# Kernel optimization log

Measured on AMD Instinct MI355X. Metric: run time of the kernel, lower is better.

Reference implementation:

```python
import jax, jax.numpy as jnp
import numpy as np

B, T, C = 4, 2048, 1024
HEADS = 16
HEAD_DIM = C // HEADS
WINDOW = 256


def setup_inputs() -> dict:
    key = jax.random.key(0)
    k1, k2, k3 = jax.random.split(key, 3)
    x = jax.random.normal(k1, (B, T, C), dtype=jnp.float32)
    # torch nn.Linear weights: [out_features, in_features]; scale like kaiming-uniform-ish
    W_qkv = jax.random.normal(k2, (3 * C, C), dtype=jnp.float32) * (1.0 / np.sqrt(C))
    W_proj = jax.random.normal(k3, (C, C), dtype=jnp.float32) * (1.0 / np.sqrt(C))
    return {"x": x, "W_qkv": W_qkv, "W_proj": W_proj}


def reference(x, W_qkv, W_proj):
    b, t, c = x.shape
    h, d = HEADS, HEAD_DIM
    qkv = x @ W_qkv.T  # [b,t,3c]
    q, k, v = jnp.split(qkv, 3, axis=-1)
    q = q.reshape(b, t, h, d).transpose(0, 2, 1, 3)  # [b,h,t,d]
    k = k.reshape(b, t, h, d).transpose(0, 2, 1, 3)
    v = v.reshape(b, t, h, d).transpose(0, 2, 1, 3)
    scale = 1.0 / jnp.sqrt(jnp.asarray(d, dtype=q.dtype))
    scores = jnp.einsum('bhqd,bhkd->bhqk', q, k) * scale  # [b,h,t,t]
    i = jnp.arange(t)[:, None]
    j = jnp.arange(t)[None, :]
    mask = (j <= i) & (j > i - WINDOW)  # sliding-window causal band
    scores = jnp.where(mask, scores, -jnp.inf)
    attn = jax.nn.softmax(scores, axis=-1)
    y = jnp.einsum('bhqk,bhkd->bhqd', attn, v)  # [b,h,t,d]
    y = y.transpose(0, 2, 1, 3).reshape(b, t, c)
    return y @ W_proj.T
```

## Files before the change

kernel.cpp:

```cpp
#include <hip/hip_runtime.h>
#include <hip/hip_bf16.h>
#include <math.h>

#define BB 4
#define TT 2048
#define CC 1024
#define HH 16
#define DD 64
#define WW 256
#define MM (BB*TT)
#define NX (MM*CC)
#define NQ (3*CC*CC)
#define NP (CC*CC)

typedef __bf16 bf16x8 __attribute__((ext_vector_type(8)));
typedef __bf16 bf16x4 __attribute__((ext_vector_type(4)));
typedef float  f32x4  __attribute__((ext_vector_type(4)));

__device__ __forceinline__ void async_cp16(const void* g, void* l) {
  __builtin_amdgcn_global_load_lds(
      (const __attribute__((address_space(1))) void*)g,
      (__attribute__((address_space(3))) void*)l, 16, 0, 0);
}

__device__ __forceinline__ unsigned short f2bf(float v) {
  __hip_bfloat16 h = __float2bfloat16(v);
  return *(unsigned short*)&h;
}

__device__ __forceinline__ size_t wpk_off(int n, int k) {
  return ((((size_t)(n >> 7) * 16 + (k >> 6)) * 16) +
          (((k >> 3) & 7) * 2 + ((n >> 6) & 1))) * 512 +
         (size_t)(n & 63) * 8 + (k & 7);
}

__global__ __launch_bounds__(256)
void prep(const float* __restrict__ x,
          const float* __restrict__ wq,
          const float* __restrict__ wp,
          unsigned short* __restrict__ wpk,
          unsigned short* __restrict__ Apk) {
  const int p = blockIdx.x;
  const int tid = threadIdx.x;
  if (p < 4096) {
    int i = (p * 256 + tid) * 4;
    const float* src; unsigned short* dst; int n, k;
    if (i < NQ) { src = wq + i; n = i >> 10; k = i & 1023; dst = wpk; }
    else {
      int j = i - NQ;
      src = wp + j; n = j >> 10; k = j & 1023; dst = wpk + NQ;
    }
    float4 v = *(const float4*)src;
    size_t off = wpk_off(n, k);
    dst[off + 0] = f2bf(v.x);
    dst[off + 1] = f2bf(v.y);
    dst[off + 2] = f2bf(v.z);
    dst[off + 3] = f2bf(v.w);
    return;
  }
  __shared__ __align__(16) unsigned short tile[64 * 72];
  const int pid = p - 4096;
  const int bm = pid & 127;
  const int bk = pid >> 7;
  const int tr = tid >> 4;
  const int tc = (tid & 15) * 4;
#pragma unroll
  for (int i = 0; i < 4; i++) {
    int row = i * 16 + tr;
    float4 v = *(const float4*)&x[(size_t)(bm * 64 + row) * 1024 + bk * 64 + tc];
    tile[row * 72 + tc + 0] = f2bf(v.x);
    tile[row * 72 + tc + 1] = f2bf(v.y);
    tile[row * 72 + tc + 2] = f2bf(v.z);
    tile[row * 72 + tc + 3] = f2bf(v.w);
  }
  __syncthreads();
  const int w = tid >> 6, lane = tid & 63;
  const int quad = lane >> 4, l15 = lane & 15;
#pragma unroll
  for (int f = 0; f < 2; f++) {
    bf16x8 fr = *(const bf16x8*)&tile[(w * 16 + l15) * 72 + f * 32 + quad * 8];
    *(bf16x8*)&Apk[(((size_t)(bm * 4 + w) * 32) + bk * 2 + f) * 512 + lane * 8] = fr;
  }
}

__global__ __launch_bounds__(256, 2)
void gemm_qkv(const unsigned short* __restrict__ Apk,
              const unsigned short* __restrict__ Bw,
              unsigned short* __restrict__ Qh,
              unsigned short* __restrict__ Kh,
              unsigned short* __restrict__ Vt) {
  __shared__ __align__(16) unsigned short Bs[4][8192];

  const int id   = blockIdx.x;
  const int xcd  = id & 7;
  const int slot = id >> 3;
  const int mloc = slot / 24;
  const int nloc = slot % 24;
  const int m0 = (xcd * 4 + mloc) * 256;
  const int n0 = nloc * 128;

  const int tid  = threadIdx.x;
  const int w    = tid >> 6;
  const int lane = tid & 63;
  const int quad = lane >> 4;
  const int l15  = lane & 15;

  f32x4 acc[4][8];
#pragma unroll
  for (int i = 0; i < 4; i++)
#pragma unroll
    for (int j = 0; j < 8; j++) acc[i][j] = (f32x4)0.0f;

  const unsigned short* abase =
      Apk + ((size_t)((m0 >> 4) + w * 4) * 32) * 512 + lane * 8;

  const unsigned short* wb = Bw + (size_t)(n0 >> 7) * (16 * 16 * 512);

  auto stageB = [&](int kt, unsigned short* bs) {
#pragma unroll
    for (int i = 0; i < 4; i++) {
      int idx = w + 4 * i;
      async_cp16(wb + ((size_t)kt * 16 + idx) * 512 + lane * 8,
                 &bs[idx * 512]);
    }
  };

  bf16x8 Af[3][4];
  auto loadA = [&](int g, bf16x8* fr) {
#pragma unroll
    for (int tm = 0; tm < 4; tm++)
      fr[tm] = *(const bf16x8*)(abase + ((size_t)(tm * 32 + g)) * 512);
  };

  loadA(0, Af[0]);
  loadA(1, Af[1]);
  stageB(0, Bs[0]);
  stageB(1, Bs[1]);
  stageB(2, Bs[2]);
  asm volatile("s_waitcnt vmcnt(0)" ::: "memory");
  __builtin_amdgcn_sched_barrier(0);
  asm volatile("s_barrier" ::: "memory");

#pragma unroll
  for (int s = 0; s < 16; s++) {
    const unsigned short* bs = Bs[s & 3];
    if (s + 3 < 16) stageB(s + 3, Bs[(s + 3) & 3]);
#pragma unroll
    for (int sub = 0; sub < 2; sub++) {
      const int g = s * 2 + sub;
      if (g + 2 < 32) loadA(g + 2, Af[(g + 2) % 3]);
      const bf16x8* af = Af[g % 3];
      __builtin_amdgcn_s_setprio(1);
#pragma unroll
      for (int tn = 0; tn < 8; tn++) {
        bf16x8 bfv = *(const bf16x8*)
            &bs[(sub * 4 + quad) * 1024 + (tn * 16 + l15) * 8];
#pragma unroll
        for (int tm = 0; tm < 4; tm++)
          acc[tm][tn] = __builtin_amdgcn_mfma_f32_16x16x32_bf16(
              af[tm], bfv, acc[tm][tn], 0, 0, 0);
      }
      __builtin_amdgcn_s_setprio(0);
    }
    asm volatile("s_waitcnt vmcnt(16) lgkmcnt(0)" ::: "memory");
    __builtin_amdgcn_sched_barrier(0);
    asm volatile("s_barrier" ::: "memory");
  }

  const int t3 = n0 >> 10;
  if (t3 == 0) {
#pragma unroll
    for (int tm = 0; tm < 4; tm++)
#pragma unroll
      for (int tn = 0; tn < 8; tn++) {
        int colb = n0 + tn * 16;
        int hh = (colb >> 6) & 15;
        int dd = (colb & 63) + l15;
#pragma unroll
        for (int r = 0; r < 4; r++) {
          int row = m0 + w * 64 + tm * 16 + quad * 4 + r;
          int b = row >> 11, tt = row & 2047;
          Qh[((size_t)((b * 16 + hh) * 2048 + tt)) * 64 + dd] =
              f2bf(acc[tm][tn][r] * 0.125f);
        }
      }
  } else if (t3 == 1) {
#pragma unroll
    for (int tm = 0; tm < 4; tm++)
#pragma unroll
      for (int tn = 0; tn < 8; tn++) {
        int colb = n0 + tn * 16;
        int hh = (colb >> 6) & 15;
        int dd = (colb & 63) + l15;
#pragma unroll
        for (int r = 0; r < 4; r++) {
          int row = m0 + w * 64 + tm * 16 + quad * 4 + r;
          int b = row >> 11, tt = row & 2047;
          Kh[((((size_t)(b * 16 + hh) * 32 + (tt >> 6)) * 8 + (dd >> 3)) * 512)
             + (tt & 63) * 8 + (dd & 7)] = f2bf(acc[tm][tn][r]);
        }
      }
  } else {
    unsigned short* T = &Bs[0][0] + w * 4608;
    const int b    = (m0 + w * 64) >> 11;
    const int tc_g = ((m0 & 2047) >> 6) + w;
    const int h0   = (n0 >> 6) & 15;
#pragma unroll
    for (int hp = 0; hp < 2; hp++) {
#pragma unroll
      for (int tnl = 0; tnl < 4; tnl++)
#pragma unroll
        for (int tm = 0; tm < 4; tm++)
#pragma unroll
          for (int r = 0; r < 4; r++)
            T[(tnl * 16 + l15) * 72 + tm * 16 + quad * 4 + r] =
                f2bf(acc[tm][hp * 4 + tnl][r]);
      asm volatile("s_waitcnt lgkmcnt(0)" ::: "memory");
      const size_t base =
          ((size_t)((b * 16 + h0 + hp) * 32 + tc_g)) * 4096;
#pragma unroll
      for (int j = 0; j < 8; j++) {
        bf16x8 v = *(const bf16x8*)&T[lane * 72 + j * 8];
        *(bf16x8*)&Vt[base + (size_t)j * 512 + lane * 8] = v;
      }
    }
  }
}

__global__ __launch_bounds__(256, 2)
void gemm_proj(const unsigned short* __restrict__ Apk,
               const unsigned short* __restrict__ Bw,
               float* __restrict__ Co) {
  __shared__ __align__(16) unsigned short Bs[4][8192];

  const int id   = blockIdx.x;
  const int xcd  = id & 7;
  const int slot = id >> 3;
  const int mloc = slot >> 3;
  const int nloc = slot & 7;
  const int m0 = (xcd * 8 + mloc) * 128;
  const int n0 = nloc * 128;

  const int tid  = threadIdx.x;
  const int w    = tid >> 6;
  const int lane = tid & 63;
  const int quad = lane >> 4;
  const int l15  = lane & 15;

  f32x4 acc[2][8];
#pragma unroll
  for (int i = 0; i < 2; i++)
#pragma unroll
    for (int j = 0; j < 8; j++) acc[i][j] = (f32x4)0.0f;

  const unsigned short* abase =
      Apk + ((size_t)((m0 >> 4) + w * 2) * 32) * 512 + lane * 8;

  const unsigned short* wb = Bw + (size_t)(n0 >> 7) * (16 * 16 * 512);

  auto stageB = [&](int kt, unsigned short* bs) {
#pragma unroll
    for (int i = 0; i < 4; i++) {
      int idx = w + 4 * i;
      async_cp16(wb + ((size_t)kt * 16 + idx) * 512 + lane * 8,
                 &bs[idx * 512]);
    }
  };

  bf16x8 Af[3][2];
  auto loadA = [&](int g, bf16x8* fr) {
#pragma unroll
    for (int tm = 0; tm < 2; tm++)
      fr[tm] = *(const bf16x8*)(abase + ((size_t)(tm * 32 + g)) * 512);
  };

  stageB(0, Bs[0]);
  stageB(1, Bs[1]);
  stageB(2, Bs[2]);
  loadA(0, Af[0]);
  loadA(1, Af[1]);
  asm volatile("s_waitcnt vmcnt(12)" ::: "memory");
  __builtin_amdgcn_sched_barrier(0);
  __builtin_amdgcn_s_barrier();

#pragma unroll
  for (int s = 0; s < 16; s++) {
    const unsigned short* bs = Bs[s & 3];
    unsigned short* bn = Bs[(s + 3) & 3];
#pragma unroll
    for (int ph = 0; ph < 4; ph++) {
      const int ksub = ph >> 1;
      const int th   = ph & 1;
      const int g    = s * 2 + ksub;
      bf16x8 bfv[4];
#pragma unroll
      for (int j = 0; j < 4; j++)
        bfv[j] = *(const bf16x8*)
            &bs[(ksub * 4 + quad) * 1024 + ((th * 4 + j) * 16 + l15) * 8];
      if (s + 3 < 16)
        async_cp16(wb + ((size_t)(s + 3) * 16 + (w + 4 * ph)) * 512 + lane * 8,
                   &bn[(w + 4 * ph) * 512]);
      if ((ph & 1) == 0 && g + 2 < 32) loadA(g + 2, Af[(g + 2) % 3]);
      __builtin_amdgcn_s_barrier();
      asm volatile("s_waitcnt lgkmcnt(0)" ::: "memory");
      __builtin_amdgcn_sched_barrier(0);
      const bf16x8* af = Af[g % 3];
      __builtin_amdgcn_s_setprio(1);
#pragma unroll
      for (int j = 0; j < 4; j++)
#pragma unroll
        for (int tm = 0; tm < 2; tm++)
          acc[tm][th * 4 + j] = __builtin_amdgcn_mfma_f32_16x16x32_bf16(
              af[tm], bfv[j], acc[tm][th * 4 + j], 0, 0, 0);
      __builtin_amdgcn_s_setprio(0);
      __builtin_amdgcn_sched_barrier(0);
      if (ph == 3 && s < 15) {
        if (s <= 12)      asm volatile("s_waitcnt vmcnt(16)" ::: "memory");
        else if (s == 13) asm volatile("s_waitcnt vmcnt(12)" ::: "memory");
        else              asm volatile("s_waitcnt vmcnt(8)"  ::: "memory");
        __builtin_amdgcn_sched_barrier(0);
      }
      __builtin_amdgcn_s_barrier();
    }
  }

#pragma unroll
  for (int tm = 0; tm < 2; tm++)
#pragma unroll
    for (int tn = 0; tn < 8; tn++)
#pragma unroll
      for (int r = 0; r < 4; r++) {
        int row = m0 + w * 32 + tm * 16 + quad * 4 + r;
        int col = n0 + tn * 16 + l15;
        Co[(size_t)row * 1024 + col] = acc[tm][tn][r];
      }
}

__global__ __launch_bounds__(256, 2)
void attn_mfma(const unsigned short* __restrict__ Qh,
               const unsigned short* __restrict__ Kh,
               const unsigned short* __restrict__ Vt,
               unsigned short* __restrict__ Ypk) {
  __shared__ __align__(16) unsigned short SH[40960];

  const int tid  = threadIdx.x;
  const int w    = tid >> 6;
  const int lane = tid & 63;
  const int quad = lane >> 4;
  const int l15  = lane & 15;

  const int vid  = blockIdx.y * 32 + blockIdx.x;
  const int v    = (vid & 7) * 256 + (vid >> 3);
  const int bh   = v >> 5;
  const int q0   = (v & 31) << 6;

  const int c0 = (q0 >= 256) ? 0 : (4 - (q0 >> 6));

  const unsigned short* Qg = Qh + ((size_t)bh * 2048 + q0) * 64;
  bf16x8 Qf[2];
#pragma unroll
  for (int fs = 0; fs < 2; fs++)
    Qf[fs] = *(const bf16x8*)(Qg + (w * 16 + l15) * 64 + fs * 32 + quad * 8);

  const unsigned short* Kg = Kh + (size_t)bh * 32 * 4096;
  const unsigned short* Vg = Vt + (size_t)bh * 32 * 4096;
  for (int ch = c0; ch < 5; ch++) {
    int tc = (q0 >> 6) - 4 + ch;
#pragma unroll
    for (int i = 0; i < 2; i++) {
      int kc = w * 2 + i;
      async_cp16(Kg + ((size_t)tc * 8 + kc) * 512 + lane * 8,
                 &SH[ch * 4096 + kc * 512]);
    }
  }
  for (int ch = c0; ch < 5; ch++) {
    int tc = (q0 >> 6) - 4 + ch;
#pragma unroll
    for (int i = 0; i < 2; i++) {
      int kc = w * 2 + i;
      async_cp16(Vg + ((size_t)tc * 8 + kc) * 512 + lane * 8,
                 &SH[20480 + ch * 4096 + kc * 512]);
    }
  }
  if (c0 == 0)      asm volatile("s_waitcnt vmcnt(10)" ::: "memory");
  else if (c0 == 1) asm volatile("s_waitcnt vmcnt(8)"  ::: "memory");
  else if (c0 == 2) asm volatile("s_waitcnt vmcnt(6)"  ::: "memory");
  else if (c0 == 3) asm volatile("s_waitcnt vmcnt(4)"  ::: "memory");
  else              asm volatile("s_waitcnt vmcnt(2)"  ::: "memory");
  __builtin_amdgcn_sched_barrier(0);
  asm volatile("s_barrier" ::: "memory");

  f32x4 S[5][4];
#pragma unroll
  for (int ch = 0; ch < 5; ch++)
#pragma unroll
    for (int tn = 0; tn < 4; tn++) S[ch][tn] = (f32x4)0.0f;

#pragma unroll
  for (int ch = 0; ch < 5; ch++) {
    if (ch < c0) continue;
#pragma unroll
    for (int ks = 0; ks < 2; ks++) {
      int kc = ks * 4 + quad;
#pragma unroll
      for (int tn = 0; tn < 4; tn++) {
        bf16x8 bk = *(const bf16x8*)
            &SH[ch * 4096 + kc * 512 + (tn * 16 + l15) * 8];
        S[ch][tn] = __builtin_amdgcn_mfma_f32_16x16x32_bf16(
            Qf[ks], bk, S[ch][tn], 0, 0, 0);
      }
    }
  }

  const int qb = q0 + w * 16 + quad * 4;
  if (c0 == 0) {
#pragma unroll
    for (int tn = 0; tn < 4; tn++) {
      int j = q0 - 256 + tn * 16 + l15;
#pragma unroll
      for (int r = 0; r < 4; r++)
        if (qb + r > j + (WW - 1)) S[0][tn][r] = -__builtin_inff();
    }
  }
#pragma unroll
  for (int tn = 0; tn < 4; tn++) {
    int j = q0 + tn * 16 + l15;
#pragma unroll
    for (int r = 0; r < 4; r++)
      if (j > qb + r) S[4][tn][r] = -__builtin_inff();
  }

  float mrow[4], lrow[4];
#pragma unroll
  for (int r = 0; r < 4; r++) mrow[r] = -__builtin_inff();
#pragma unroll
  for (int ch = 0; ch < 5; ch++) {
    if (ch < c0) continue;
#pragma unroll
    for (int tn = 0; tn < 4; tn++)
#pragma unroll
      for (int r = 0; r < 4; r++)
        mrow[r] = fmaxf(mrow[r], S[ch][tn][r]);
  }
#pragma unroll
  for (int off = 1; off < 16; off <<= 1)
#pragma unroll
    for (int r = 0; r < 4; r++)
      mrow[r] = fmaxf(mrow[r], __shfl_xor(mrow[r], off));

#pragma unroll
  for (int r = 0; r < 4; r++) lrow[r] = 0.0f;
#pragma unroll
  for (int ch = 0; ch < 5; ch++) {
    if (ch < c0) continue;
#pragma unroll
    for (int tn = 0; tn < 4; tn++)
#pragma unroll
      for (int r = 0; r < 4; r++) {
        float e = __expf(S[ch][tn][r] - mrow[r]);
        S[ch][tn][r] = e;
        lrow[r] += e;
      }
  }
#pragma unroll
  for (int off = 1; off < 16; off <<= 1)
#pragma unroll
    for (int r = 0; r < 4; r++) lrow[r] += __shfl_xor(lrow[r], off);

  asm volatile("s_waitcnt vmcnt(0)" ::: "memory");
  __builtin_amdgcn_sched_barrier(0);
  asm volatile("s_barrier" ::: "memory");

  f32x4 Oacc[4];
#pragma unroll
  for (int td = 0; td < 4; td++) Oacc[td] = (f32x4)0.0f;

#pragma unroll
  for (int ch = 0; ch < 5; ch++) {
    if (ch < c0) continue;
    unsigned short* Ps = SH + (ch & 1) * 4608;
#pragma unroll
    for (int tn = 0; tn < 4; tn++)
#pragma unroll
      for (int r = 0; r < 4; r++)
        Ps[(w * 16 + quad * 4 + r) * 68 + tn * 16 + l15] = f2bf(S[ch][tn][r]);
    asm volatile("s_waitcnt lgkmcnt(0)" ::: "memory");
#pragma unroll
    for (int ks = 0; ks < 2; ks++) {
      int off = (w * 16 + l15) * 68 + ks * 32 + quad * 8;
      bf16x4 plo = *(const bf16x4*)&Ps[off];
      bf16x4 phi = *(const bf16x4*)&Ps[off + 4];
      bf16x8 ap = __builtin_shufflevector(plo, phi, 0, 1, 2, 3, 4, 5, 6, 7);
      int kc = ks * 4 + quad;
#pragma unroll
      for (int td = 0; td < 4; td++) {
        bf16x8 bv = *(const bf16x8*)
            &SH[20480 + ch * 4096 + kc * 512 + (td * 16 + l15) * 8];
        Oacc[td] = __builtin_amdgcn_mfma_f32_16x16x32_bf16(
            ap, bv, Oacc[td], 0, 0, 0);
      }
    }
  }

  const int b = bh >> 4, h = bh & 15;
  float inv[4];
#pragma unroll
  for (int r = 0; r < 4; r++) inv[r] = 1.0f / lrow[r];
  unsigned short* Ot = SH + 10240;
#pragma unroll
  for (int td = 0; td < 4; td++)
#pragma unroll
    for (int r = 0; r < 4; r++)
      Ot[(w * 16 + quad * 4 + r) * 72 + td * 16 + l15] =
          f2bf(Oacc[td][r] * inv[r]);
  asm volatile("s_waitcnt lgkmcnt(0)" ::: "memory");
  const size_t rt = (size_t)((b * 2048 + q0) >> 4) + w;
#pragma unroll
  for (int f = 0; f < 2; f++) {
    bf16x8 fr = *(const bf16x8*)&Ot[(w * 16 + l15) * 72 + f * 32 + quad * 8];
    *(bf16x8*)&Ypk[(rt * 32 + h * 2 + f) * 512 + lane * 8] = fr;
  }
}

extern "C" void kernel_launch(void* const* d_in, const int* in_sizes, int n_in,
                              void* d_out, int out_size, void* d_ws, size_t ws_size,
                              hipStream_t stream) {
  const float* x     = (const float*)d_in[0];
  const float* wqkv  = (const float*)d_in[1];
  const float* wproj = (const float*)d_in[2];
  float* out = (float*)d_out;

  char* ws = (char*)d_ws;
  unsigned short* apk    = (unsigned short*)(ws);
  unsigned short* wqkvb  = (unsigned short*)(ws + (size_t)16 * 1024 * 1024);
  unsigned short* wprojb = (unsigned short*)(ws + (size_t)22 * 1024 * 1024);
  unsigned short* qh     = (unsigned short*)(ws + (size_t)24 * 1024 * 1024);
  unsigned short* kh     = (unsigned short*)(ws + (size_t)40 * 1024 * 1024);
  unsigned short* vt     = (unsigned short*)(ws + (size_t)56 * 1024 * 1024);
  unsigned short* ypk    = (unsigned short*)(ws + (size_t)72 * 1024 * 1024);

  prep<<<4096 + 2048, 256, 0, stream>>>(x, wqkv, wproj, wqkvb, apk);

  gemm_qkv<<<768, 256, 0, stream>>>(apk, wqkvb, qh, kh, vt);

  attn_mfma<<<dim3(TT / 64, BB * HH), 256, 0, stream>>>(
      qh, kh, vt, ypk);

  gemm_proj<<<512, 256, 0, stream>>>(ypk, wprojb, out);
}
```

Before: 200.6 us.

## Stream K/V chunks through ring buffers to cut attention LDS footprint

The attention kernel no longer stages all five K and V chunks in shared memory up front. K now uses a double buffer and V a triple buffer, each refilled inside the QK and PV loops with vmcnt waits and barriers per chunk. LDS use drops from about 80KB to about 50KB, which is meant to allow more resident blocks and to overlap loads with MFMA work. In exchange it adds many more block barriers, and it issues clamped dummy loads for chunks that are out of range so the vmcnt counts stay uniform.

Result: no change. 198.1 us (-1.2%).

```diff
diff --git a/kernel.cpp b/kernel.cpp
--- a/kernel.cpp
+++ b/kernel.cpp
@@ -341,7 +341,7 @@
                const unsigned short* __restrict__ Kh,
                const unsigned short* __restrict__ Vt,
                unsigned short* __restrict__ Ypk) {
-  __shared__ __align__(16) unsigned short SH[40960];
+  __shared__ __align__(16) unsigned short SH[25088];
 
   const int tid  = threadIdx.x;
   const int w    = tid >> 6;
@@ -353,7 +353,6 @@
   const int v    = (vid & 7) * 256 + (vid >> 3);
   const int bh   = v >> 5;
   const int q0   = (v & 31) << 6;
-
   const int c0 = (q0 >= 256) ? 0 : (4 - (q0 >> 6));
 
   const unsigned short* Qg = Qh + ((size_t)bh * 2048 + q0) * 64;
@@ -361,34 +360,34 @@
 #pragma unroll
   for (int fs = 0; fs < 2; fs++)
     Qf[fs] = *(const bf16x8*)(Qg + (w * 16 + l15) * 64 + fs * 32 + quad * 8);
+  __builtin_amdgcn_sched_barrier(0);
 
   const unsigned short* Kg = Kh + (size_t)bh * 32 * 4096;
   const unsigned short* Vg = Vt + (size_t)bh * 32 * 4096;
-  for (int ch = c0; ch < 5; ch++) {
-    int tc = (q0 >> 6) - 4 + ch;
+
+  auto tcc = [&](int ch) { int t = (q0 >> 6) - 4 + ch; return t < 0 ? 0 : t; };
+  auto stageK = [&](int ch) {
+    int t = tcc(ch);
 #pragma unroll
     for (int i = 0; i < 2; i++) {
       int kc = w * 2 + i;
-      async_cp16(Kg + ((size_t)tc * 8 + kc) * 512 + lane * 8,
-                 &SH[ch * 4096 + kc * 512]);
-    }
-  }
-  for (int ch = c0; ch < 5; ch++) {
-    int tc = (q0 >> 6) - 4 + ch;
+      async_cp16(Kg + ((size_t)t * 8 + kc) * 512 + lane * 8,
+                 &SH[(ch & 1) * 4096 + kc * 512]);
+    }
+  };
+  auto stageV = [&](int ch) {
+    int t = tcc(ch);
 #pragma unroll
     for (int i = 0; i < 2; i++) {
       int kc = w * 2 + i;
-      async_cp16(Vg + ((size_t)tc * 8 + kc) * 512 + lane * 8,
-                 &SH[20480 + ch * 4096 + kc * 512]);
-    }
-  }
-  if (c0 == 0)      asm volatile("s_waitcnt vmcnt(10)" ::: "memory");
-  else if (c0 == 1) asm volatile("s_waitcnt vmcnt(8)"  ::: "memory");
-  else if (c0 == 2) asm volatile("s_waitcnt vmcnt(6)"  ::: "memory");
-  else if (c0 == 3) asm volatile("s_waitcnt vmcnt(4)"  ::: "memory");
-  else              asm volatile("s_waitcnt vmcnt(2)"  ::: "memory");
+      async_cp16(Vg + ((size_t)t * 8 + kc) * 512 + lane * 8,
+                 &SH[8192 + (ch % 3) * 4096 + kc * 512]);
+    }
+  };
+
+  stageK(0); stageK(1);
+  stageV(0); stageV(1); stageV(2);
   __builtin_amdgcn_sched_barrier(0);
-  asm volatile("s_barrier" ::: "memory");
 
   f32x4 S[5][4];
 #pragma unroll
@@ -398,18 +397,28 @@
 
 #pragma unroll
   for (int ch = 0; ch < 5; ch++) {
-    if (ch < c0) continue;
-#pragma unroll
-    for (int ks = 0; ks < 2; ks++) {
-      int kc = ks * 4 + quad;
-#pragma unroll
-      for (int tn = 0; tn < 4; tn++) {
-        bf16x8 bk = *(const bf16x8*)
-            &SH[ch * 4096 + kc * 512 + (tn * 16 + l15) * 8];
-        S[ch][tn] = __builtin_amdgcn_mfma_f32_16x16x32_bf16(
-            Qf[ks], bk, S[ch][tn], 0, 0, 0);
-      }
-    }
+    if (ch <= 1)      asm volatile("s_waitcnt vmcnt(8)" ::: "memory");
+    else if (ch <= 3) asm volatile("s_waitcnt vmcnt(2)" ::: "memory");
+    else              asm volatile("s_waitcnt vmcnt(0)" ::: "memory");
+    __builtin_amdgcn_sched_barrier(0);
+    __builtin_amdgcn_s_barrier();
+    if (ch >= c0) {
+#pragma unroll
+      for (int ks = 0; ks < 2; ks++) {
+        int kc = ks * 4 + quad;
+#pragma unroll
+        for (int tn = 0; tn < 4; tn++) {
+          bf16x8 bk = *(const bf16x8*)
+              &SH[(ch & 1) * 4096 + kc * 512 + (tn * 16 + l15) * 8];
+          S[ch][tn] = __builtin_amdgcn_mfma_f32_16x16x32_bf16(
+              Qf[ks], bk, S[ch][tn], 0, 0, 0);
+        }
+      }
+    }
+    asm volatile("s_waitcnt lgkmcnt(0)" ::: "memory");
+    __builtin_amdgcn_sched_barrier(0);
+    __builtin_amdgcn_s_barrier();
+    if (ch + 2 <= 4) { stageK(ch + 2); __builtin_amdgcn_sched_barrier(0); }
   }
 
   const int qb = q0 + w * 16 + quad * 4;
@@ -467,38 +476,55 @@
 #pragma unroll
     for (int r = 0; r < 4; r++) lrow[r] += __shfl_xor(lrow[r], off);
 
-  asm volatile("s_waitcnt vmcnt(0)" ::: "memory");
-  __builtin_amdgcn_sched_barrier(0);
-  asm volatile("s_barrier" ::: "memory");
-
   f32x4 Oacc[4];
 #pragma unroll
   for (int td = 0; td < 4; td++) Oacc[td] = (f32x4)0.0f;
+  unsigned short* Ps = SH + 20480;
 
 #pragma unroll
   for (int ch = 0; ch < 5; ch++) {
-    if (ch < c0) continue;
-    unsigned short* Ps = SH + (ch & 1) * 4608;
-#pragma unroll
-    for (int tn = 0; tn < 4; tn++)
-#pragma unroll
-      for (int r = 0; r < 4; r++)
-        Ps[(w * 16 + quad * 4 + r) * 68 + tn * 16 + l15] = f2bf(S[ch][tn][r]);
-    asm volatile("s_waitcnt lgkmcnt(0)" ::: "memory");
-#pragma unroll
-    for (int ks = 0; ks < 2; ks++) {
-      int off = (w * 16 + l15) * 68 + ks * 32 + quad * 8;
-      bf16x4 plo = *(const bf16x4*)&Ps[off];
-      bf16x4 phi = *(const bf16x4*)&Ps[off + 4];
-      bf16x8 ap = __builtin_shufflevector(plo, phi, 0, 1, 2, 3, 4, 5, 6, 7);
-      int kc = ks * 4 + quad;
-#pragma unroll
-      for (int td = 0; td < 4; td++) {
-        bf16x8 bv = *(const bf16x8*)
-            &SH[20480 + ch * 4096 + kc * 512 + (td * 16 + l15) * 8];
-        Oacc[td] = __builtin_amdgcn_mfma_f32_16x16x32_bf16(
-            ap, bv, Oacc[td], 0, 0, 0);
-      }
+    if (ch == 3) {
+      asm volatile("s_waitcnt vmcnt(2)" ::: "memory");
+      __builtin_amdgcn_sched_barrier(0);
+      __builtin_amdgcn_s_barrier();
+    } else if (ch == 4) {
+      asm volatile("s_waitcnt vmcnt(0)" ::: "memory");
+      __builtin_amdgcn_sched_barrier(0);
+      __builtin_amdgcn_s_barrier();
+    }
+    if (ch >= c0) {
+      asm volatile("s_waitcnt lgkmcnt(0)" ::: "memory");
+#pragma unroll
+      for (int tn = 0; tn < 4; tn++)
+#pragma unroll
+        for (int r = 0; r < 4; r++)
+          Ps[(w * 16 + quad * 4 + r) * 68 + tn * 16 + l15] = f2bf(S[ch][tn][r]);
+      asm volatile("s_waitcnt lgkmcnt(0)" ::: "memory");
+      __builtin_amdgcn_sched_barrier(0);
+#pragma unroll
+      for (int ks = 0; ks < 2; ks++) {
+        int off = (w * 16 + l15) * 68 + ks * 32 + quad * 8;
+        bf16x4 plo = *(const bf16x4*)&Ps[off];
+        bf16x4 phi = *(const bf16x4*)&Ps[off + 4];
+        bf16x8 ap = __builtin_shufflevector(plo, phi, 0, 1, 2, 3, 4, 5, 6, 7);
+        int kc = ks * 4 + quad;
+#pragma unroll
+        for (int td = 0; td < 4; td++) {
+          bf16x8 bv = *(const bf16x8*)
+              &SH[8192 + (ch % 3) * 4096 + kc * 512 + (td * 16 + l15) * 8];
+          Oacc[td] = __builtin_amdgcn_mfma_f32_16x16x32_bf16(
+              ap, bv, Oacc[td], 0, 0, 0);
+        }
+      }
+    }
+    if (ch == 0) {
+      asm volatile("s_waitcnt lgkmcnt(0)" ::: "memory");
+      __builtin_amdgcn_s_barrier();
+      stageV(3); __builtin_amdgcn_sched_barrier(0);
+    } else if (ch == 1) {
+      asm volatile("s_waitcnt lgkmcnt(0)" ::: "memory");
+      __builtin_amdgcn_s_barrier();
+      stageV(4); __builtin_amdgcn_sched_barrier(0);
     }
   }
 
@@ -506,18 +532,18 @@
   float inv[4];
 #pragma unroll
   for (int r = 0; r < 4; r++) inv[r] = 1.0f / lrow[r];
-  unsigned short* Ot = SH + 10240;
+  unsigned short* Ot = SH + 20480;
 #pragma unroll
   for (int td = 0; td < 4; td++)
 #pragma unroll
     for (int r = 0; r < 4; r++)
-      Ot[(w * 16 + quad * 4 + r) * 72 + td * 16 + l15] =
+      Ot[(w * 16 + quad * 4 + r) * 68 + td * 16 + l15] =
           f2bf(Oacc[td][r] * inv[r]);
   asm volatile("s_waitcnt lgkmcnt(0)" ::: "memory");
   const size_t rt = (size_t)((b * 2048 + q0) >> 4) + w;
 #pragma unroll
   for (int f = 0; f < 2; f++) {
-    bf16x8 fr = *(const bf16x8*)&Ot[(w * 16 + l15) * 72 + f * 32 + quad * 8];
+    bf16x8 fr = *(const bf16x8*)&Ot[(w * 16 + l15) * 68 + f * 32 + quad * 8];
     *(bf16x8*)&Ypk[(rt * 32 + h * 2 + f) * 512 + lane * 8] = fr;
   }
 }
```
